# Optimization experiments

Measured on AMD Instinct MI355X. Metric: run time of the kernel, lower is better.

The kernel has to match this reference:

```python
import jax, jax.numpy as jnp
import numpy as np

B, S, IN, H, Q, M, K = 32, 2048, 128, 256, 16, 64, 3


def setup_inputs() -> dict:
    key = jax.random.key(0)
    ks = jax.random.split(key, 12)
    rn = lambda k, shp, s=0.05: (jax.random.normal(k, shp, jnp.float32) * s)
    return {
        "input_sequence": rn(ks[0], (B, S, IN), 1.0),
        "W_ih0": rn(ks[1], (4 * H, IN)),
        "W_hh0": rn(ks[2], (4 * H, H)),
        "b_ih0": jnp.zeros((4 * H,), jnp.float32),
        "b_hh0": jnp.zeros((4 * H,), jnp.float32),
        "W_ih1": rn(ks[3], (4 * H, H)),
        "W_hh1": rn(ks[4], (4 * H, H)),
        "b_ih1": jnp.zeros((4 * H,), jnp.float32),
        "b_hh1": jnp.zeros((4 * H,), jnp.float32),
        "W_cq": rn(ks[5], (Q, H)),
        "b_cq": jnp.zeros((Q,), jnp.float32),
        "mem_keys": rn(ks[6], (M, Q), 1.0),
        "mem_vals": rn(ks[7], (M, H), 1.0),
        "W_out": rn(ks[8], (H, 2 * H)),
        "b_out": jnp.zeros((H,), jnp.float32),
        "classical_weight": jnp.float32(0.7),
        "quantum_weight": jnp.float32(0.3),
    }


def _lstm_layer(x, W_ih, W_hh, b_ih, b_hh):
    """PyTorch-convention LSTM layer (gate order i,f,g,o), batch_first input."""
    Bb = x.shape[0]
    Hh = W_hh.shape[1]
    # precompute the input contribution for all timesteps: [B,S,4H]
    xg = jnp.einsum('bsi,gi->bsg', x, W_ih) + b_ih + b_hh

    def step(carry, xt):
        h, c = carry
        g = xt + h @ W_hh.T  # [B,4H]
        i, f, gg, o = jnp.split(g, 4, axis=-1)
        i = jax.nn.sigmoid(i)
        f = jax.nn.sigmoid(f)
        gg = jnp.tanh(gg)
        o = jax.nn.sigmoid(o)
        c = f * c + i * gg
        h = o * jnp.tanh(c)
        return (h, c), h

    init = (jnp.zeros((Bb, Hh), x.dtype), jnp.zeros((Bb, Hh), x.dtype))
    _, hs = jax.lax.scan(step, init, jnp.swapaxes(xg, 0, 1))  # [S,B,H]
    return jnp.swapaxes(hs, 0, 1)


def _forward(input_sequence, W_ih0, W_hh0, b_ih0, b_hh0, W_ih1, W_hh1, b_ih1,
             b_hh1, W_cq, b_cq, mem_keys, mem_vals, W_out, b_out,
             classical_weight, quantum_weight):
    # classical 2-layer LSTM
    h1 = _lstm_layer(input_sequence, W_ih0, W_hh0, b_ih0, b_hh0)
    lstm_out = _lstm_layer(h1, W_ih1, W_hh1, b_ih1, b_hh1)  # [B,S,H]

    # classical_to_quantum + tanh -> per-token query [B,S,Q]
    q = jnp.tanh(jnp.einsum('bsh,qh->bsq', lstm_out, W_cq) + b_cq)

    # batched k-NN read over the quantum memory (cosine similarity, k=3)
    eps = jnp.float32(1e-8)
    qn = q / (jnp.linalg.norm(q, axis=-1, keepdims=True) + eps)
    kn = mem_keys / (jnp.linalg.norm(mem_keys, axis=-1, keepdims=True) + eps)
    sims = jnp.einsum('bsq,mq->bsm', qn, kn)          # [B,S,M]
    top_vals, top_idx = jax.lax.top_k(sims, K)        # [B,S,K]
    gathered = mem_vals[top_idx]                      # [B,S,K,H]

    # similarity-weighted average of retrieved contents
    tot = jnp.sum(top_vals, axis=-1, keepdims=True)   # [B,S,1]
    weighted = jnp.einsum('bsk,bskh->bsh', top_vals, gathered)
    enhanced = jnp.where(tot > 0, weighted / jnp.where(tot == 0, 1.0, tot), 0.0)

    # combine streams and project
    combined = jnp.concatenate(
        [classical_weight * lstm_out, quantum_weight * enhanced], axis=-1)
    out = jnp.einsum('bsc,hc->bsh', combined, W_out) + b_out  # [B,S,H]
    return out


def reference(input_sequence, W_ih0, W_hh0, b_ih0, b_hh0, W_ih1, W_hh1, b_ih1,
              b_hh1, W_cq, b_cq, mem_keys, mem_vals, W_out, b_out,
              classical_weight, quantum_weight):
    return _forward(input_sequence, W_ih0, W_hh0, b_ih0, b_hh0, W_ih1, W_hh1,
                    b_ih1, b_hh1, W_cq, b_cq, mem_keys, mem_vals, W_out, b_out,
                    classical_weight, quantum_weight)
```

## Files before the change

### kernel.cpp

```cpp
#include <hip/hip_runtime.h>
#include <cstdint>
#include <cstddef>
#include <math.h>

#define B_   32
#define S_   2048
#define IN_  128
#define H_   256
#define Q_   16
#define M_   64
#define D_   4

typedef unsigned long long u64;
typedef __attribute__((ext_vector_type(4))) unsigned int u32x4;

__device__ __forceinline__ float4 ld4(const float* p) { return *(const float4*)p; }

#define AGLD64(p)    __hip_atomic_load((p),  __ATOMIC_RELAXED, __HIP_MEMORY_SCOPE_AGENT)
#define AGST64(p, v) __hip_atomic_store((p), (v), __ATOMIC_RELAXED, __HIP_MEMORY_SCOPE_AGENT)

__device__ __forceinline__ u32x4 mall_load_2x64(const u64* p) {
  u32x4 q;
  asm volatile("global_load_dwordx4 %0, %1, off sc0 sc1\n\ts_waitcnt vmcnt(0)"
               : "=v"(q) : "v"(p) : "memory");
  return q;
}

__device__ __forceinline__ float sigm_f(float x) { return 1.0f / (1.0f + __expf(-x)); }
__device__ __forceinline__ float tanh_f(float x) { return 1.0f - 2.0f / (__expf(2.0f * x) + 1.0f); }

__global__ __launch_bounds__(256, 1) void lstm2(
    const float* __restrict__ x,
    const float* __restrict__ Wih0, const float* __restrict__ bih0,
    const float* __restrict__ bhh0, const float* __restrict__ Whh0,
    const float* __restrict__ Wih1, const float* __restrict__ bih1,
    const float* __restrict__ bhh1, const float* __restrict__ Whh1,
    float* __restrict__ out,
    u64* __restrict__ exs)
{
  const int f = blockIdx.x;
  const int n = f >> 5;
  const int b = f & 31;

  const int tid = threadIdx.x;
  const int w   = tid >> 6;
  const int l   = tid & 63;
  const int kc  = l & 7;
  const int rg  = l >> 3;
  const int wrg = w * 8 + rg;
  const int col = n * 32 + wrg;

  __shared__ float w1[128][257];
  __shared__ float aring[8][256];
  __shared__ float hring[2][256];
  __shared__ float x_sh[2][IN_];

#pragma unroll
  for (int s2 = 0; s2 < 8; s2++) aring[s2][tid] = 0.0f;
  hring[0][tid] = 0.0f;
  hring[1][tid] = 0.0f;

  float4 wf0[4][8], wf1[4][8], wi0[4][4];
  float rb0[4], rb1[4];
#pragma unroll
  for (int g = 0; g < 4; g++) {
    const int row = g * 256 + col;
    const float* p0 = Whh0 + (size_t)row * 256 + 4 * kc;
    const float* p1 = Whh1 + (size_t)row * 256 + 4 * kc;
    const float* pi = Wih0 + (size_t)row * 128 + 4 * kc;
#pragma unroll
    for (int j = 0; j < 8; j++) {
      wf0[g][j] = ld4(p0 + 32 * j);
      wf1[g][j] = ld4(p1 + 32 * j);
    }
#pragma unroll
    for (int j = 0; j < 4; j++) wi0[g][j] = ld4(pi + 32 * j);
    rb0[g] = bih0[row] + bhh0[row];
    rb1[g] = bih1[row] + bhh1[row];
    const float* pw = Wih1 + (size_t)row * 256 + 4 * kc;
    float* dst = &w1[g * 32 + wrg][4 * kc];
#pragma unroll
    for (int j = 0; j < 8; j++) *(float4*)(dst + 32 * j) = ld4(pw + 32 * j);
  }

  const float* xrow = x + (size_t)b * S_ * IN_;
  float* outp = out + (size_t)b * S_ * H_;
  u64* sexb = exs + (size_t)b * 1024;

  if (tid < IN_) {
    x_sh[0][tid] = xrow[tid];
    x_sh[1][tid] = xrow[IN_ + tid];
  }
  float xreg = (tid < IN_) ? xrow[(size_t)2 * IN_ + tid] : 0.0f;
  float cst0 = 0.0f, cst1 = 0.0f;
  float xa0s[4], xa1s[4] = {0, 0, 0, 0};
  __syncthreads();

  {
    const float* xb = x_sh[0];
    float4 xv[4];
#pragma unroll
    for (int j = 0; j < 4; j++) xv[j] = ld4(xb + 4 * kc + 32 * j);
#pragma unroll
    for (int g = 0; g < 4; g++) {
      float4 s4 = {0, 0, 0, 0};
#pragma unroll
      for (int j = 0; j < 4; j++) {
        s4.x += wi0[g][j].x * xv[j].x; s4.y += wi0[g][j].y * xv[j].y;
        s4.z += wi0[g][j].z * xv[j].z; s4.w += wi0[g][j].w * xv[j].w;
      }
      float s = (s4.x + s4.y) + (s4.z + s4.w);
      s += __shfl_xor(s, 1); s += __shfl_xor(s, 2); s += __shfl_xor(s, 4);
      xa0s[g] = s + rb0[g];
    }
  }

  bool dead = false;
  for (int t = 0; t < S_ + D_; ++t) {
    const bool doA = (t < S_);
    const int  u   = t - D_;
    const bool doH = (u >= 0);
    const int  pa = t & 1, ph = u & 1;
    const unsigned eA = (unsigned)(t + 1), eH = (unsigned)(u + 1);

    float xreg_n = 0.0f;
    if (tid < IN_ && t + 2 < S_) {
      int tn = (t + 3 < S_) ? t + 3 : S_ - 1;
      xreg_n = xrow[(size_t)tn * IN_ + tid];
    }

    if (doA) {
      const float* ap = aring[(t - 1) & 7];
      float4 av[8];
#pragma unroll
      for (int j = 0; j < 8; j++) av[j] = ld4(ap + 4 * kc + 32 * j);
      float gv[4];
#pragma unroll
      for (int g = 0; g < 4; g++) {
        float4 s4 = {0, 0, 0, 0};
#pragma unroll
        for (int j = 0; j < 8; j++) {
          s4.x += wf0[g][j].x * av[j].x; s4.y += wf0[g][j].y * av[j].y;
          s4.z += wf0[g][j].z * av[j].z; s4.w += wf0[g][j].w * av[j].w;
        }
        float s = (s4.x + s4.y) + (s4.z + s4.w);
        s += __shfl_xor(s, 1); s += __shfl_xor(s, 2); s += __shfl_xor(s, 4);
        gv[g] = s + xa0s[g];
      }
      float ig = sigm_f(gv[0]);
      float fg = sigm_f(gv[1]);
      float cg = tanh_f(gv[2]);
      float og = sigm_f(gv[3]);
      cst0 = fg * cst0 + ig * cg;
      float a = og * tanh_f(cst0);
      if (kc == 0) {
        u64 pk = ((u64)eA << 32) | (u64)__float_as_uint(a);
        AGST64(sexb + ((0 * 2 + pa) << 8) + col, pk);
        aring[t & 7][col] = a;
      }
    }
    if (doH) {
      const float* hp = hring[(t - 1) & 1];
      float4 hv[8];
#pragma unroll
      for (int j = 0; j < 8; j++) hv[j] = ld4(hp + 4 * kc + 32 * j);
      float gv[4];
#pragma unroll
      for (int g = 0; g < 4; g++) {
        float4 s4 = {0, 0, 0, 0};
#pragma unroll
        for (int j = 0; j < 8; j++) {
          s4.x += wf1[g][j].x * hv[j].x; s4.y += wf1[g][j].y * hv[j].y;
          s4.z += wf1[g][j].z * hv[j].z; s4.w += wf1[g][j].w * hv[j].w;
        }
        float s = (s4.x + s4.y) + (s4.z + s4.w);
        s += __shfl_xor(s, 1); s += __shfl_xor(s, 2); s += __shfl_xor(s, 4);
        gv[g] = s + xa1s[g];
      }
      float ig = sigm_f(gv[0]);
      float fg = sigm_f(gv[1]);
      float cg = tanh_f(gv[2]);
      float og = sigm_f(gv[3]);
      cst1 = fg * cst1 + ig * cg;
      float h = og * tanh_f(cst1);
      if (kc == 0) {
        outp[(size_t)u * H_ + col] = h;
        u64 pk = ((u64)eH << 32) | (u64)__float_as_uint(h);
        AGST64(sexb + ((1 * 2 + ph) << 8) + col, pk);
        hring[u & 1][col] = h;
      }
    }

    if (t + 1 < S_) {
      const float* xb = x_sh[(t + 1) & 1];
      float4 xv[4];
#pragma unroll
      for (int j = 0; j < 4; j++) xv[j] = ld4(xb + 4 * kc + 32 * j);
#pragma unroll
      for (int g = 0; g < 4; g++) {
        float4 s4 = {0, 0, 0, 0};
#pragma unroll
        for (int j = 0; j < 4; j++) {
          s4.x += wi0[g][j].x * xv[j].x; s4.y += wi0[g][j].y * xv[j].y;
          s4.z += wi0[g][j].z * xv[j].z; s4.w += wi0[g][j].w * xv[j].w;
        }
        float s = (s4.x + s4.y) + (s4.z + s4.w);
        s += __shfl_xor(s, 1); s += __shfl_xor(s, 2); s += __shfl_xor(s, 4);
        xa0s[g] = s + rb0[g];
      }
    }
    {
      const int v = t - D_ + 1;
      if (v >= 0 && v < S_) {
        const float* avp = aring[v & 7];
        float4 av[8];
#pragma unroll
        for (int j = 0; j < 8; j++) av[j] = ld4(avp + 4 * kc + 32 * j);
#pragma unroll
        for (int g = 0; g < 4; g++) {
          const float* wr = &w1[g * 32 + wrg][4 * kc];
          float4 s4 = {0, 0, 0, 0};
#pragma unroll
          for (int j = 0; j < 8; j++) {
            float4 wv = ld4(wr + 32 * j);
            s4.x += wv.x * av[j].x; s4.y += wv.y * av[j].y;
            s4.z += wv.z * av[j].z; s4.w += wv.w * av[j].w;
          }
          float s = (s4.x + s4.y) + (s4.z + s4.w);
          s += __shfl_xor(s, 1); s += __shfl_xor(s, 2); s += __shfl_xor(s, 4);
          xa1s[g] = s + rb1[g];
        }
      }
    }

    {
      const bool isA = (tid < 128);
      const int  pi2 = isA ? tid : tid - 128;
      const bool ownp = ((pi2 >> 4) == n);
      const bool act  = isA ? doA : doH;
      bool need = act && !ownp && !dead;
      if (need) {
        const unsigned etag = isA ? eA : eH;
        const int plane = isA ? (0 * 2 + pa) : (1 * 2 + ph);
        u64* base = sexb + (plane << 8) + 2 * pi2;
        unsigned val0 = 0, val1 = 0;
        bool got = false;
#pragma unroll 1
        for (int it = 0; it < 16 && !got; ++it) {
          u32x4 q = mall_load_2x64(base);
          if (q.y == etag && q.w == etag) { val0 = q.x; val1 = q.z; got = true; }
        }
        if (!got) {
          bool g0 = false, g1 = false;
          unsigned guard = 0;
          while (!(g0 && g1)) {
            if (!g0) { u64 v = AGLD64(base);     if ((unsigned)(v >> 32) == etag) { val0 = (unsigned)v; g0 = true; } }
            if (!g1) { u64 v = AGLD64(base + 1); if ((unsigned)(v >> 32) == etag) { val1 = (unsigned)v; g1 = true; } }
            if (++guard >= (1u << 20)) { dead = true; break; }
          }
        }
        float2 f2;
        f2.x = __uint_as_float(val0);
        f2.y = __uint_as_float(val1);
        if (isA) *(float2*)&aring[t & 7][2 * pi2] = f2;
        else     *(float2*)&hring[u & 1][2 * pi2] = f2;
      }
    }

    if (tid < IN_ && t < S_) x_sh[t & 1][tid] = xreg;
    xreg = xreg_n;
    __syncthreads();
  }
}

__global__ __launch_bounds__(256) void knn_enh(
    const float* __restrict__ lstm, const float* __restrict__ Wcq,
    const float* __restrict__ bcq, const float* __restrict__ keys,
    const float* __restrict__ vals, const float* __restrict__ qwp,
    float* __restrict__ enh)
{
  const int tid  = threadIdx.x;
  const int wave = tid >> 6, lane = tid & 63;
  const int t = blockIdx.x * 4 + wave;

  __shared__ float xsh[4][256];
  __shared__ float qsh[4][16];

  const float* xrow = lstm + (size_t)t * H_;
  float4 x4 = ld4(xrow + lane * 4);
  *(float4*)&xsh[wave][lane * 4] = x4;
  __syncthreads();

  const int j = lane & 15, seg = lane >> 4;
  const float* wrow = Wcq + j * H_ + seg * 64;
  const float* xseg = &xsh[wave][seg * 64];
  float p = 0.0f;
#pragma unroll
  for (int c = 0; c < 64; c += 4) {
    float4 w4 = ld4(wrow + c);
    p += w4.x * xseg[c] + w4.y * xseg[c + 1] + w4.z * xseg[c + 2] + w4.w * xseg[c + 3];
  }
  p += __shfl_xor(p, 16);
  p += __shfl_xor(p, 32);
  float q = tanhf(p + bcq[j]);

  float sq = q * q;
  sq += __shfl_xor(sq, 1); sq += __shfl_xor(sq, 2);
  sq += __shfl_xor(sq, 4); sq += __shfl_xor(sq, 8);
  float qn = q / (sqrtf(sq) + 1e-8f);
  if (lane < 16) qsh[wave][lane] = qn;
  __syncthreads();

  const int m = lane;
  const float* krow = keys + m * Q_;
  float kv[16]; float kn2 = 0.0f;
#pragma unroll
  for (int jj = 0; jj < 16; jj++) { kv[jj] = krow[jj]; kn2 += kv[jj] * kv[jj]; }
  float rn = 1.0f / (sqrtf(kn2) + 1e-8f);
  float sim = 0.0f;
#pragma unroll
  for (int jj = 0; jj < 16; jj++) sim += qsh[wave][jj] * kv[jj];
  sim *= rn;

  float rem = sim;
  float tv[3]; int ti[3];
#pragma unroll
  for (int k = 0; k < 3; k++) {
    float v = rem; int idx = m;
#pragma unroll
    for (int d = 1; d < 64; d <<= 1) {
      float ov = __shfl_xor(v, d);
      int   oi = __shfl_xor(idx, d);
      if (ov > v || (ov == v && oi < idx)) { v = ov; idx = oi; }
    }
    tv[k] = v; ti[k] = idx;
    if (m == idx) rem = -INFINITY;
  }
  float tot = tv[0] + tv[1] + tv[2];

  float ex = 0, ey = 0, ez = 0, ew = 0;
#pragma unroll
  for (int k = 0; k < 3; k++) {
    float4 vv = ld4(vals + (size_t)ti[k] * H_ + lane * 4);
    ex += tv[k] * vv.x; ey += tv[k] * vv.y;
    ez += tv[k] * vv.z; ew += tv[k] * vv.w;
  }
  float inv = (tot > 0.0f) ? 1.0f / tot : 0.0f;
  const float qw = qwp[0];

  float4 o;
  o.x = qw * ex * inv; o.y = qw * ey * inv;
  o.z = qw * ez * inv; o.w = qw * ew * inv;
  *(float4*)&enh[(size_t)t * H_ + lane * 4] = o;
}

__global__ __launch_bounds__(256) void gemm_cat(
    float* __restrict__ io, const float* __restrict__ A2,
    const float* __restrict__ Bw, const float* __restrict__ bias,
    const float* __restrict__ cwp)
{
  __shared__ float As[16][68];
  __shared__ float Bs[16][260];
  const int tid  = threadIdx.x;
  const int row0 = blockIdx.x * 64;
  const int tx = tid & 15, ty = tid >> 4;
  const int lr = tid >> 2;
  const int lk = (tid & 3) << 2;
  const float cw = cwp[0];

  float acc[4][16];
#pragma unroll
  for (int i = 0; i < 4; i++)
#pragma unroll
    for (int j = 0; j < 16; j++) acc[i][j] = 0.0f;

  for (int k0 = 0; k0 < 512; k0 += 16) {
    float4 av;
    if (k0 < 256) {
      av = ld4(io + (size_t)(row0 + lr) * 256 + k0 + lk);
      av.x *= cw; av.y *= cw; av.z *= cw; av.w *= cw;
    } else {
      av = ld4(A2 + (size_t)(row0 + lr) * 256 + (k0 - 256) + lk);
    }
    As[lk + 0][lr] = av.x; As[lk + 1][lr] = av.y;
    As[lk + 2][lr] = av.z; As[lk + 3][lr] = av.w;
    const float* bp = Bw + (size_t)tid * 512 + k0;
#pragma unroll
    for (int q = 0; q < 4; q++) {
      float4 b4 = ld4(bp + 4 * q);
      Bs[4 * q + 0][tid] = b4.x; Bs[4 * q + 1][tid] = b4.y;
      Bs[4 * q + 2][tid] = b4.z; Bs[4 * q + 3][tid] = b4.w;
    }
    __syncthreads();
#pragma unroll
    for (int k = 0; k < 16; k++) {
      float4 a4 = *(const float4*)&As[k][ty << 2];
      float aa[4] = {a4.x, a4.y, a4.z, a4.w};
#pragma unroll
      for (int cc = 0; cc < 4; cc++) {
        float4 b4 = *(const float4*)&Bs[k][cc * 64 + (tx << 2)];
        float bb[4] = {b4.x, b4.y, b4.z, b4.w};
#pragma unroll
        for (int i = 0; i < 4; i++)
#pragma unroll
          for (int jj = 0; jj < 4; jj++) acc[i][cc * 4 + jj] += aa[i] * bb[jj];
      }
    }
    __syncthreads();
  }

#pragma unroll
  for (int i = 0; i < 4; i++) {
#pragma unroll
    for (int cc = 0; cc < 4; cc++) {
      int c0 = cc * 64 + (tx << 2);
      float4 o;
      o.x = acc[i][cc * 4 + 0] + bias[c0 + 0];
      o.y = acc[i][cc * 4 + 1] + bias[c0 + 1];
      o.z = acc[i][cc * 4 + 2] + bias[c0 + 2];
      o.w = acc[i][cc * 4 + 3] + bias[c0 + 3];
      *(float4*)&io[(size_t)(row0 + (ty << 2) + i) * 256 + c0] = o;
    }
  }
}

extern "C" void kernel_launch(void* const* d_in, const int* in_sizes, int n_in,
                              void* d_out, int out_size, void* d_ws, size_t ws_size,
                              hipStream_t stream)
{
  const float* x    = (const float*)d_in[0];
  const float* Wih0 = (const float*)d_in[1];
  const float* Whh0 = (const float*)d_in[2];
  const float* bih0 = (const float*)d_in[3];
  const float* bhh0 = (const float*)d_in[4];
  const float* Wih1 = (const float*)d_in[5];
  const float* Whh1 = (const float*)d_in[6];
  const float* bih1 = (const float*)d_in[7];
  const float* bhh1 = (const float*)d_in[8];
  const float* Wcq  = (const float*)d_in[9];
  const float* bcq  = (const float*)d_in[10];
  const float* keys = (const float*)d_in[11];
  const float* vals = (const float*)d_in[12];
  const float* Wout = (const float*)d_in[13];
  const float* bout = (const float*)d_in[14];
  const float* cw   = (const float*)d_in[15];
  const float* qw   = (const float*)d_in[16];
  float* out = (float*)d_out;

  const size_t HE = (size_t)B_ * S_ * H_;
  if (ws_size < HE * sizeof(float)) return;
  u64* exs = (u64*)d_ws;
  float* enh = (float*)d_ws;

  const int MT = B_ * S_;
  dim3 blk(256);

  hipMemsetAsync(exs, 0, (size_t)32 * 1024 * sizeof(u64), stream);
  lstm2<<<dim3(256), blk, 0, stream>>>(x, Wih0, bih0, bhh0, Whh0,
                                       Wih1, bih1, bhh1, Whh1, out, exs);

  knn_enh<<<dim3(MT / 4), blk, 0, stream>>>(out, Wcq, bcq, keys, vals, qw, enh);

  gemm_cat<<<dim3(MT / 64), blk, 0, stream>>>(out, enh, Wout, bout, cw);
}
```

Before: 13.57 ms.

## Double LSTM block width, regroup batch blocks, and prefetch exchange loads early

The recurrent LSTM kernel now runs 512 threads per block, so 16 lanes share each gate row's dot product instead of 8. That halves the per-thread weight registers and adds one more shuffle-reduction step. Block indexing is changed so the 8 column-slice blocks of one batch row get consecutive block IDs, which may change how they are placed across the chip and how fast they exchange data. The cross-block hidden-state exchange now uses one 64-bit value per thread, issued before the input-projection work and waited on afterwards, to hide the polling latency. The activation ring buffer also shrinks from 8 to 4 slots.

Measured after the change: 13.05 ms. -3.8%, faster.

```diff
diff --git a/kernel.cpp b/kernel.cpp
--- a/kernel.cpp
+++ b/kernel.cpp
@@ -12,24 +12,31 @@
 #define D_   4
 
 typedef unsigned long long u64;
-typedef __attribute__((ext_vector_type(4))) unsigned int u32x4;
+typedef __attribute__((ext_vector_type(2))) unsigned int u32x2;
 
 __device__ __forceinline__ float4 ld4(const float* p) { return *(const float4*)p; }
 
 #define AGLD64(p)    __hip_atomic_load((p),  __ATOMIC_RELAXED, __HIP_MEMORY_SCOPE_AGENT)
 #define AGST64(p, v) __hip_atomic_store((p), (v), __ATOMIC_RELAXED, __HIP_MEMORY_SCOPE_AGENT)
 
-__device__ __forceinline__ u32x4 mall_load_2x64(const u64* p) {
-  u32x4 q;
-  asm volatile("global_load_dwordx4 %0, %1, off sc0 sc1\n\ts_waitcnt vmcnt(0)"
+__device__ __forceinline__ u32x2 mall_load_u64(const u64* p) {
+  u32x2 q;
+  asm volatile("global_load_dwordx2 %0, %1, off sc0 sc1\n\ts_waitcnt vmcnt(0)"
                : "=v"(q) : "v"(p) : "memory");
   return q;
 }
+__device__ __forceinline__ void mall_issue1(const u64* p, u32x2& q) {
+  asm volatile("global_load_dwordx2 %0, %1, off sc0 sc1"
+               : "=&v"(q) : "v"(p) : "memory");
+}
+__device__ __forceinline__ void mall_wait1(u32x2& q) {
+  asm volatile("s_waitcnt vmcnt(0)" : "+v"(q) :: "memory");
+}
 
 __device__ __forceinline__ float sigm_f(float x) { return 1.0f / (1.0f + __expf(-x)); }
 __device__ __forceinline__ float tanh_f(float x) { return 1.0f - 2.0f / (__expf(2.0f * x) + 1.0f); }
 
-__global__ __launch_bounds__(256, 1) void lstm2(
+__global__ __launch_bounds__(512, 1) void lstm2(
     const float* __restrict__ x,
     const float* __restrict__ Wih0, const float* __restrict__ bih0,
     const float* __restrict__ bhh0, const float* __restrict__ Whh0,
@@ -39,28 +46,26 @@
     u64* __restrict__ exs)
 {
   const int f = blockIdx.x;
-  const int n = f >> 5;
-  const int b = f & 31;
+  const int n = f & 7;
+  const int b = f >> 3;
 
   const int tid = threadIdx.x;
   const int w   = tid >> 6;
   const int l   = tid & 63;
-  const int kc  = l & 7;
-  const int rg  = l >> 3;
-  const int wrg = w * 8 + rg;
+  const int kc  = l & 15;
+  const int rg  = l >> 4;
+  const int wrg = w * 4 + rg;
   const int col = n * 32 + wrg;
 
   __shared__ float w1[128][257];
-  __shared__ float aring[8][256];
+  __shared__ float aring[4][256];
   __shared__ float hring[2][256];
   __shared__ float x_sh[2][IN_];
 
-#pragma unroll
-  for (int s2 = 0; s2 < 8; s2++) aring[s2][tid] = 0.0f;
-  hring[0][tid] = 0.0f;
-  hring[1][tid] = 0.0f;
-
-  float4 wf0[4][8], wf1[4][8], wi0[4][4];
+  for (int i = tid; i < 4 * 256; i += 512) ((float*)aring)[i] = 0.0f;
+  for (int i = tid; i < 2 * 256; i += 512) ((float*)hring)[i] = 0.0f;
+
+  float4 wf0[4][4], wf1[4][4], wi0[4][2];
   float rb0[4], rb1[4];
 #pragma unroll
   for (int g = 0; g < 4; g++) {
@@ -69,23 +74,23 @@
     const float* p1 = Whh1 + (size_t)row * 256 + 4 * kc;
     const float* pi = Wih0 + (size_t)row * 128 + 4 * kc;
 #pragma unroll
-    for (int j = 0; j < 8; j++) {
-      wf0[g][j] = ld4(p0 + 32 * j);
-      wf1[g][j] = ld4(p1 + 32 * j);
-    }
-#pragma unroll
-    for (int j = 0; j < 4; j++) wi0[g][j] = ld4(pi + 32 * j);
+    for (int j = 0; j < 4; j++) {
+      wf0[g][j] = ld4(p0 + 64 * j);
+      wf1[g][j] = ld4(p1 + 64 * j);
+    }
+#pragma unroll
+    for (int j = 0; j < 2; j++) wi0[g][j] = ld4(pi + 64 * j);
     rb0[g] = bih0[row] + bhh0[row];
     rb1[g] = bih1[row] + bhh1[row];
     const float* pw = Wih1 + (size_t)row * 256 + 4 * kc;
     float* dst = &w1[g * 32 + wrg][4 * kc];
 #pragma unroll
-    for (int j = 0; j < 8; j++) *(float4*)(dst + 32 * j) = ld4(pw + 32 * j);
+    for (int j = 0; j < 4; j++) *(float4*)(dst + 64 * j) = ld4(pw + 64 * j);
   }
 
   const float* xrow = x + (size_t)b * S_ * IN_;
   float* outp = out + (size_t)b * S_ * H_;
-  u64* sexb = exs + (size_t)b * 1024;
+  u64* exb = exs + (size_t)b * 1024;
 
   if (tid < IN_) {
     x_sh[0][tid] = xrow[tid];
@@ -98,19 +103,20 @@
 
   {
     const float* xb = x_sh[0];
-    float4 xv[4];
-#pragma unroll
-    for (int j = 0; j < 4; j++) xv[j] = ld4(xb + 4 * kc + 32 * j);
+    float4 xv[2];
+#pragma unroll
+    for (int j = 0; j < 2; j++) xv[j] = ld4(xb + 4 * kc + 64 * j);
 #pragma unroll
     for (int g = 0; g < 4; g++) {
       float4 s4 = {0, 0, 0, 0};
 #pragma unroll
-      for (int j = 0; j < 4; j++) {
+      for (int j = 0; j < 2; j++) {
         s4.x += wi0[g][j].x * xv[j].x; s4.y += wi0[g][j].y * xv[j].y;
         s4.z += wi0[g][j].z * xv[j].z; s4.w += wi0[g][j].w * xv[j].w;
       }
       float s = (s4.x + s4.y) + (s4.z + s4.w);
-      s += __shfl_xor(s, 1); s += __shfl_xor(s, 2); s += __shfl_xor(s, 4);
+      s += __shfl_xor(s, 1); s += __shfl_xor(s, 2);
+      s += __shfl_xor(s, 4); s += __shfl_xor(s, 8);
       xa0s[g] = s + rb0[g];
     }
   }
@@ -130,141 +136,138 @@
     }
 
     if (doA) {
-      const float* ap = aring[(t - 1) & 7];
-      float4 av[8];
-#pragma unroll
-      for (int j = 0; j < 8; j++) av[j] = ld4(ap + 4 * kc + 32 * j);
+      const float* ap = aring[(t - 1) & 3];
+      float4 av[4];
+#pragma unroll
+      for (int j = 0; j < 4; j++) av[j] = ld4(ap + 4 * kc + 64 * j);
       float gv[4];
 #pragma unroll
       for (int g = 0; g < 4; g++) {
         float4 s4 = {0, 0, 0, 0};
 #pragma unroll
-        for (int j = 0; j < 8; j++) {
+        for (int j = 0; j < 4; j++) {
           s4.x += wf0[g][j].x * av[j].x; s4.y += wf0[g][j].y * av[j].y;
           s4.z += wf0[g][j].z * av[j].z; s4.w += wf0[g][j].w * av[j].w;
         }
         float s = (s4.x + s4.y) + (s4.z + s4.w);
-        s += __shfl_xor(s, 1); s += __shfl_xor(s, 2); s += __shfl_xor(s, 4);
+        s += __shfl_xor(s, 1); s += __shfl_xor(s, 2);
+        s += __shfl_xor(s, 4); s += __shfl_xor(s, 8);
         gv[g] = s + xa0s[g];
       }
-      float ig = sigm_f(gv[0]);
-      float fg = sigm_f(gv[1]);
-      float cg = tanh_f(gv[2]);
-      float og = sigm_f(gv[3]);
+      float ig = sigm_f(gv[0]), fg = sigm_f(gv[1]);
+      float cg = tanh_f(gv[2]), og = sigm_f(gv[3]);
       cst0 = fg * cst0 + ig * cg;
       float a = og * tanh_f(cst0);
       if (kc == 0) {
         u64 pk = ((u64)eA << 32) | (u64)__float_as_uint(a);
-        AGST64(sexb + ((0 * 2 + pa) << 8) + col, pk);
-        aring[t & 7][col] = a;
+        AGST64(exb + (pa << 8) + col, pk);
+        aring[t & 3][col] = a;
       }
     }
     if (doH) {
-      const float* hp = hring[(t - 1) & 1];
-      float4 hv[8];
-#pragma unroll
-      for (int j = 0; j < 8; j++) hv[j] = ld4(hp + 4 * kc + 32 * j);
+      const float* hp = hring[(u - 1) & 1];
+      float4 hv[4];
+#pragma unroll
+      for (int j = 0; j < 4; j++) hv[j] = ld4(hp + 4 * kc + 64 * j);
       float gv[4];
 #pragma unroll
       for (int g = 0; g < 4; g++) {
         float4 s4 = {0, 0, 0, 0};
 #pragma unroll
-        for (int j = 0; j < 8; j++) {
+        for (int j = 0; j < 4; j++) {
           s4.x += wf1[g][j].x * hv[j].x; s4.y += wf1[g][j].y * hv[j].y;
           s4.z += wf1[g][j].z * hv[j].z; s4.w += wf1[g][j].w * hv[j].w;
         }
         float s = (s4.x + s4.y) + (s4.z + s4.w);
-        s += __shfl_xor(s, 1); s += __shfl_xor(s, 2); s += __shfl_xor(s, 4);
+        s += __shfl_xor(s, 1); s += __shfl_xor(s, 2);
+        s += __shfl_xor(s, 4); s += __shfl_xor(s, 8);
         gv[g] = s + xa1s[g];
       }
-      float ig = sigm_f(gv[0]);
-      float fg = sigm_f(gv[1]);
-      float cg = tanh_f(gv[2]);
-      float og = sigm_f(gv[3]);
+      float ig = sigm_f(gv[0]), fg = sigm_f(gv[1]);
+      float cg = tanh_f(gv[2]), og = sigm_f(gv[3]);
       cst1 = fg * cst1 + ig * cg;
       float h = og * tanh_f(cst1);
       if (kc == 0) {
+        u64 pk = ((u64)eH << 32) | (u64)__float_as_uint(h);
+        AGST64(exb + ((2 + ph) << 8) + col, pk);
         outp[(size_t)u * H_ + col] = h;
-        u64 pk = ((u64)eH << 32) | (u64)__float_as_uint(h);
-        AGST64(sexb + ((1 * 2 + ph) << 8) + col, pk);
         hring[u & 1][col] = h;
       }
     }
+
+    const bool isA = (tid < 256);
+    const int  e   = tid & 255;
+    const bool ownp = ((e >> 5) == n);
+    const bool act  = isA ? doA : doH;
+    const bool need = act && !ownp && !dead;
+    const unsigned etag = isA ? eA : eH;
+    const int plane = isA ? pa : 2 + ph;
+    u64* bp = exb + (plane << 8) + e;
+    u32x2 q;
+    if (need) mall_issue1(bp, q);
 
     if (t + 1 < S_) {
       const float* xb = x_sh[(t + 1) & 1];
-      float4 xv[4];
-#pragma unroll
-      for (int j = 0; j < 4; j++) xv[j] = ld4(xb + 4 * kc + 32 * j);
+      float4 xv[2];
+#pragma unroll
+      for (int j = 0; j < 2; j++) xv[j] = ld4(xb + 4 * kc + 64 * j);
 #pragma unroll
       for (int g = 0; g < 4; g++) {
         float4 s4 = {0, 0, 0, 0};
 #pragma unroll
-        for (int j = 0; j < 4; j++) {
+        for (int j = 0; j < 2; j++) {
           s4.x += wi0[g][j].x * xv[j].x; s4.y += wi0[g][j].y * xv[j].y;
           s4.z += wi0[g][j].z * xv[j].z; s4.w += wi0[g][j].w * xv[j].w;
         }
         float s = (s4.x + s4.y) + (s4.z + s4.w);
-        s += __shfl_xor(s, 1); s += __shfl_xor(s, 2); s += __shfl_xor(s, 4);
+        s += __shfl_xor(s, 1); s += __shfl_xor(s, 2);
+        s += __shfl_xor(s, 4); s += __shfl_xor(s, 8);
         xa0s[g] = s + rb0[g];
       }
     }
     {
       const int v = t - D_ + 1;
       if (v >= 0 && v < S_) {
-        const float* avp = aring[v & 7];
-        float4 av[8];
-#pragma unroll
-        for (int j = 0; j < 8; j++) av[j] = ld4(avp + 4 * kc + 32 * j);
+        const float* avp = aring[v & 3];
+        float4 av[4];
+#pragma unroll
+        for (int j = 0; j < 4; j++) av[j] = ld4(avp + 4 * kc + 64 * j);
 #pragma unroll
         for (int g = 0; g < 4; g++) {
           const float* wr = &w1[g * 32 + wrg][4 * kc];
           float4 s4 = {0, 0, 0, 0};
 #pragma unroll
-          for (int j = 0; j < 8; j++) {
-            float4 wv = ld4(wr + 32 * j);
+          for (int j = 0; j < 4; j++) {
+            float4 wv = ld4(wr + 64 * j);
             s4.x += wv.x * av[j].x; s4.y += wv.y * av[j].y;
             s4.z += wv.z * av[j].z; s4.w += wv.w * av[j].w;
           }
           float s = (s4.x + s4.y) + (s4.z + s4.w);
-          s += __shfl_xor(s, 1); s += __shfl_xor(s, 2); s += __shfl_xor(s, 4);
+          s += __shfl_xor(s, 1); s += __shfl_xor(s, 2);
+          s += __shfl_xor(s, 4); s += __shfl_xor(s, 8);
           xa1s[g] = s + rb1[g];
         }
       }
     }
 
-    {
-      const bool isA = (tid < 128);
-      const int  pi2 = isA ? tid : tid - 128;
-      const bool ownp = ((pi2 >> 4) == n);
-      const bool act  = isA ? doA : doH;
-      bool need = act && !ownp && !dead;
-      if (need) {
-        const unsigned etag = isA ? eA : eH;
-        const int plane = isA ? (0 * 2 + pa) : (1 * 2 + ph);
-        u64* base = sexb + (plane << 8) + 2 * pi2;
-        unsigned val0 = 0, val1 = 0;
-        bool got = false;
+    if (need) {
+      mall_wait1(q);
+      bool got = (q.y == etag);
 #pragma unroll 1
-        for (int it = 0; it < 16 && !got; ++it) {
-          u32x4 q = mall_load_2x64(base);
-          if (q.y == etag && q.w == etag) { val0 = q.x; val1 = q.z; got = true; }
+      for (int it = 0; it < 16 && !got; ++it) {
+        q = mall_load_u64(bp);
+        got = (q.y == etag);
+      }
+      if (!got) {
+        unsigned guard = 0;
+        while (!got) {
+          u64 v2 = AGLD64(bp);
+          if ((unsigned)(v2 >> 32) == etag) { q.x = (unsigned)v2; got = true; }
+          if (++guard >= (1u << 20)) { dead = true; break; }
         }
-        if (!got) {
-          bool g0 = false, g1 = false;
-          unsigned guard = 0;
-          while (!(g0 && g1)) {
-            if (!g0) { u64 v = AGLD64(base);     if ((unsigned)(v >> 32) == etag) { val0 = (unsigned)v; g0 = true; } }
-            if (!g1) { u64 v = AGLD64(base + 1); if ((unsigned)(v >> 32) == etag) { val1 = (unsigned)v; g1 = true; } }
-            if (++guard >= (1u << 20)) { dead = true; break; }
-          }
-        }
-        float2 f2;
-        f2.x = __uint_as_float(val0);
-        f2.y = __uint_as_float(val1);
-        if (isA) *(float2*)&aring[t & 7][2 * pi2] = f2;
-        else     *(float2*)&hring[u & 1][2 * pi2] = f2;
-      }
+      }
+      if (isA) aring[t & 3][e] = __uint_as_float(q.x);
+      else     hring[u & 1][e] = __uint_as_float(q.x);
     }
 
     if (tid < IN_ && t < S_) x_sh[t & 1][tid] = xreg;
@@ -453,13 +456,12 @@
   float* enh = (float*)d_ws;
 
   const int MT = B_ * S_;
-  dim3 blk(256);
 
   hipMemsetAsync(exs, 0, (size_t)32 * 1024 * sizeof(u64), stream);
-  lstm2<<<dim3(256), blk, 0, stream>>>(x, Wih0, bih0, bhh0, Whh0,
-                                       Wih1, bih1, bhh1, Whh1, out, exs);
-
-  knn_enh<<<dim3(MT / 4), blk, 0, stream>>>(out, Wcq, bcq, keys, vals, qw, enh);
-
-  gemm_cat<<<dim3(MT / 64), blk, 0, stream>>>(out, enh, Wout, bout, cw);
-}
+  lstm2<<<dim3(256), dim3(512), 0, stream>>>(x, Wih0, bih0, bhh0, Whh0,
+                                             Wih1, bih1, bhh1, Whh1, out, exs);
+
+  knn_enh<<<dim3(MT / 4), dim3(256), 0, stream>>>(out, Wcq, bcq, keys, vals, qw, enh);
+
+  gemm_cat<<<dim3(MT / 64), dim3(256), 0, stream>>>(out, enh, Wout, bout, cw);
+}
```
